# Kernel tuning notes

Hardware: AMD Instinct MI355X
Metric: run time of the kernel (lower is better)

The kernel has to match this reference:

```python
import jax, jax.numpy as jnp
from jax import lax
import numpy as np

ANCHOR_LENGTHS = (2.0, 4.0, 6.0, 9.0, 13.0, 18.0)  # A = 6


def make_anchors_1d(Lf, anchor_lengths):
    # anchors on the feature axis: [Lf*A, 2] (start, end)
    al = jnp.asarray(anchor_lengths, dtype=jnp.float32)          # [A]
    centers = jnp.arange(Lf, dtype=jnp.float32) + 0.5            # [Lf]
    start = centers[:, None] - 0.5 * al[None, :]                 # [Lf, A]
    end = centers[:, None] + 0.5 * al[None, :]                   # [Lf, A]
    return jnp.stack([start, end], axis=-1).reshape(Lf * al.shape[0], 2)


def setup_inputs() -> dict:
    key = jax.random.key(0)
    ks = jax.random.split(key, 4)
    B, C, Lf, A = 4, 512, 8192, len(ANCHOR_LENGTHS)
    feat = jax.random.normal(ks[0], (B, C, Lf), dtype=jnp.float32)
    conv_w = jax.random.normal(ks[1], (C, C, 3), dtype=jnp.float32) * 0.02   # OIW
    conv_b = jnp.zeros((C,), dtype=jnp.float32)
    obj_w = jax.random.normal(ks[2], (A, C, 1), dtype=jnp.float32) * 0.02
    obj_b = jnp.zeros((A,), dtype=jnp.float32)
    reg_w = jax.random.normal(ks[3], (A * 2, C, 1), dtype=jnp.float32) * 0.02
    reg_b = jnp.zeros((A * 2,), dtype=jnp.float32)
    return {"feat": feat, "conv_w": conv_w, "conv_b": conv_b,
            "obj_w": obj_w, "obj_b": obj_b, "reg_w": reg_w, "reg_b": reg_b}


def reference(feat, conv_w, conv_b, obj_w, obj_b, reg_w, reg_b):
    B, C, Lf = feat.shape
    A = obj_w.shape[0]
    # 3x1 conv, padding=1 -> SAME; layout N C W / O I W
    h = lax.conv_general_dilated(feat, conv_w, window_strides=(1,),
                                 padding="SAME",
                                 dimension_numbers=("NCH", "OIH", "NCH"))
    h = jax.nn.relu(h + conv_b[None, :, None])                   # [B, C, Lf]
    # 1x1 conv heads expressed as channel contractions
    obj = jnp.einsum("bcl,ac->bal", h, obj_w[:, :, 0]) + obj_b[None, :, None]   # [B, A, Lf]
    reg = jnp.einsum("bcl,ac->bal", h, reg_w[:, :, 0]) + reg_b[None, :, None]   # [B, 2A, Lf]
    obj = obj.transpose(0, 2, 1).reshape(B, Lf * A)                              # [B, N]
    reg = reg.transpose(0, 2, 1).reshape(B, Lf, A, 2).reshape(B, Lf * A, 2)      # [B, N, 2]
    anchors = make_anchors_1d(Lf, ANCHOR_LENGTHS)                                # [N, 2]
    return obj, reg, anchors
```

## Files before the change

### kernel.cpp

```cpp
#include <hip/hip_runtime.h>
#include <stdint.h>

typedef __attribute__((ext_vector_type(8))) short short8;
typedef __attribute__((ext_vector_type(4))) float f32x4;
typedef __attribute__((ext_vector_type(4))) float float4v;
typedef __attribute__((ext_vector_type(4))) unsigned short u16x4;
typedef __attribute__((ext_vector_type(8))) unsigned short u16x8;

#define AS1 __attribute__((address_space(1)))
#define AS3 __attribute__((address_space(3)))


__device__ __forceinline__ unsigned short f2bf(float f) {
    union { float f; unsigned int u; } v; v.f = f;
    unsigned int r = v.u + 0x7fffu + ((v.u >> 16) & 1u);
    return (unsigned short)(r >> 16);
}

__constant__ float c_AL[6] = {2.f, 4.f, 6.f, 9.f, 13.f, 18.f};

__global__ __launch_bounds__(256) void prep_transpose_kernel(
    const float* __restrict__ feat, const float* __restrict__ conv_w,
    const float* __restrict__ obj_w, const float* __restrict__ reg_w,
    unsigned short* __restrict__ wAf, unsigned short* __restrict__ hwp,
    unsigned short* __restrict__ featT, float* __restrict__ out) {
    __shared__ unsigned short tile[64][68];
    unsigned int bx = blockIdx.x;
    int tid = threadIdx.x;
    if (bx < 4096u) {
        int l0 = (bx & 127) * 64, c0 = ((bx >> 7) & 7) * 64, b = bx >> 10;
        const float* fb = feat + ((size_t)b * 512 + c0) * 8192 + l0;
        #pragma unroll
        for (int it = 0; it < 4; ++it) {
            int slot = it * 256 + tid;
            int c = slot >> 4, l4 = (slot & 15) << 2;
            float4v v = *(const float4v*)(fb + (size_t)c * 8192 + l4);
            u16x4 pk;
            pk.x = f2bf(v.x); pk.y = f2bf(v.y);
            pk.z = f2bf(v.z); pk.w = f2bf(v.w);
            *(u16x4*)(&tile[c][l4]) = pk;
        }
        __syncthreads();
        unsigned short* ftb = featT + ((size_t)b * 8208 + 1 + l0) * 512 + c0;
        #pragma unroll
        for (int it = 0; it < 2; ++it) {
            int slot = it * 256 + tid;
            int l = slot >> 3, c8 = (slot & 7) << 3;
            u16x8 pk;
            #pragma unroll
            for (int j = 0; j < 8; ++j) pk[j] = tile[c8 + j][l];
            *(u16x8*)(ftb + (size_t)l * 512 + c8) = pk;
        }
        return;
    }
    unsigned int idx = (bx - 4096u) * 256 + tid;
    if (idx < 786432u) {
        unsigned int chunkid = idx >> 9;
        unsigned int within = idx & 511u;
        unsigned int lane = within >> 3, j = within & 7u;
        unsigned int kc = chunkid & 15u;
        unsigned int ct = chunkid >> 4;
        unsigned int t = ct % 3u, cb = ct / 3u;
        unsigned int cout = cb * 16u + (lane & 15u);
        unsigned int cin = kc * 32u + (lane >> 4) * 8u + j;
        wAf[idx] = f2bf(conv_w[(cout * 512u + cin) * 3u + t]);
    } else if (idx < 802816u) {
        unsigned int i2 = idx - 786432u;
        unsigned int j = i2 >> 9, c = i2 & 511u;
        float v = 0.f;
        if (j < 6u) v = obj_w[j * 512u + c];
        else if (j < 18u) v = reg_w[(j - 6u) * 512u + c];
        hwp[i2] = f2bf(v);
    } else if (idx < 851968u) {
        unsigned int n = idx - 802816u;
        unsigned int l = n / 6u, a = n - l * 6u;
        float ctr = (float)l + 0.5f, half = 0.5f * c_AL[a];
        float* anchors = out + 589824;
        anchors[2 * n]     = ctr - half;
        anchors[2 * n + 1] = ctr + half;
    } else if (idx < 856064u) {
        unsigned int i4 = idx - 851968u;
        unsigned int b = i4 >> 10, rem = i4 & 1023u;
        unsigned int row = (rem >> 9) ? 8193u : 0u;
        unsigned int c = rem & 511u;
        featT[((size_t)b * 8208 + row) * 512 + c] = 0;
    }
}

__global__ __launch_bounds__(256, 4) void conv_gemm_kernel(
    const unsigned short* __restrict__ wAf,
    const unsigned short* __restrict__ featT,
    const float* __restrict__ conv_b,
    const unsigned short* __restrict__ hwp,
    float* __restrict__ part) {
    __shared__ unsigned short smem[17408];

    const int tid = threadIdx.x;
    const int wave = tid >> 6, lane = tid & 63;
    const int lq = lane >> 4, lr = lane & 15;
    const int l0 = blockIdx.x * 128;
    const int m0 = blockIdx.y * 128;
    const int b = blockIdx.z;
    const int wm = wave >> 1, wn = wave & 1;
    const unsigned short* ftb = featT + (size_t)b * 8208 * 512;

    f32x4 acc[4][4];
    #pragma unroll
    for (int i = 0; i < 4; ++i)
        #pragma unroll
        for (int j = 0; j < 4; ++j)
            acc[i][j] = (f32x4){0.f, 0.f, 0.f, 0.f};

    for (int kc = 0; kc < 16; ++kc) {
        __syncthreads();
        for (int ci = wave; ci < 33; ci += 4) {
            const unsigned short* g;
            if (ci < 24) {
                int t = ci >> 3, rb = ci & 7;
                g = wAf + ((size_t)(((m0 >> 4) + rb) * 3 + t) * 16 + kc) * 512 + lane * 8;
            } else {
                int lb = ci - 24;
                g = ftb + (size_t)(l0 + lb * 16 + lr) * 512 + kc * 32 + lq * 8;
            }
            __builtin_amdgcn_global_load_lds((const AS1 void*)g,
                                             (AS3 void*)(smem + ci * 512), 16, 0, 0);
        }
        __syncthreads();
        #pragma unroll
        for (int t = 0; t < 3; ++t) {
            short8 af[4], bf[4];
            #pragma unroll
            for (int fm = 0; fm < 4; ++fm)
                af[fm] = *(const short8*)(smem + ((t * 8 + wm * 4 + fm) << 9) + (lane << 3));
            #pragma unroll
            for (int fn = 0; fn < 4; ++fn) {
                int R = wn * 64 + fn * 16 + lr + t;
                bf[fn] = *(const short8*)(smem + ((24 + (R >> 4)) << 9) +
                                          ((((lq << 4) | (R & 15))) << 3));
            }
            #pragma unroll
            for (int fm = 0; fm < 4; ++fm)
                #pragma unroll
                for (int fn = 0; fn < 4; ++fn)
                    acc[fm][fn] = __builtin_amdgcn_mfma_f32_16x16x32_bf16(
                        af[fm], bf[fn], acc[fm][fn], 0, 0, 0);
        }
    }
    __syncthreads();
    #pragma unroll
    for (int fm = 0; fm < 4; ++fm) {
        int mb = wm * 64 + fm * 16 + lq * 4;
        float cb0 = conv_b[m0 + mb];
        float cb1 = conv_b[m0 + mb + 1];
        float cb2 = conv_b[m0 + mb + 2];
        float cb3 = conv_b[m0 + mb + 3];
        #pragma unroll
        for (int fn = 0; fn < 4; ++fn) {
            int n = wn * 64 + fn * 16 + lr;
            f32x4 v = acc[fm][fn];
            u16x4 pk;
            pk.x = f2bf(fmaxf(v.x + cb0, 0.f));
            pk.y = f2bf(fmaxf(v.y + cb1, 0.f));
            pk.z = f2bf(fmaxf(v.z + cb2, 0.f));
            pk.w = f2bf(fmaxf(v.w + cb3, 0.f));
            *(u16x4*)(smem + n * 136 + mb) = pk;
        }
    }
    __syncthreads();
    f32x4 hacc[2][2];
    #pragma unroll
    for (int i = 0; i < 2; ++i) {
        hacc[i][0] = (f32x4){0.f, 0.f, 0.f, 0.f};
        hacc[i][1] = (f32x4){0.f, 0.f, 0.f, 0.f};
    }
    const int lbase = wave * 32;
    for (int kk = 0; kk < 4; ++kk) {
        short8 ha[2], hb2[2];
        #pragma unroll
        for (int fm2 = 0; fm2 < 2; ++fm2)
            ha[fm2] = *(const short8*)(smem + (lbase + fm2 * 16 + lr) * 136 + kk * 32 + lq * 8);
        #pragma unroll
        for (int fn = 0; fn < 2; ++fn)
            hb2[fn] = *(const short8*)(hwp + (size_t)(fn * 16 + lr) * 512 + m0 + kk * 32 + lq * 8);
        #pragma unroll
        for (int fm2 = 0; fm2 < 2; ++fm2)
            #pragma unroll
            for (int fn = 0; fn < 2; ++fn)
                hacc[fm2][fn] = __builtin_amdgcn_mfma_f32_16x16x32_bf16(
                    ha[fm2], hb2[fn], hacc[fm2][fn], 0, 0, 0);
    }
    float* pb = part + ((size_t)(blockIdx.y * 4 + b) * 8192) * 18;
    #pragma unroll
    for (int fn = 0; fn < 2; ++fn) {
        int j = fn * 16 + lr;
        if (j >= 18) continue;
        #pragma unroll
        for (int fm2 = 0; fm2 < 2; ++fm2)
            #pragma unroll
            for (int r = 0; r < 4; ++r) {
                int l = l0 + lbase + fm2 * 16 + lq * 4 + r;
                pb[(size_t)l * 18 + j] = hacc[fm2][fn][r];
            }
    }
}

__global__ __launch_bounds__(256) void reduce_kernel(
    const float* __restrict__ part, const float* __restrict__ obj_b,
    const float* __restrict__ reg_b, float* __restrict__ out) {
    unsigned int idx = blockIdx.x * 256 + threadIdx.x;
    if (idx >= 589824u) return;
    unsigned int j = idx % 18u;
    unsigned int t = idx / 18u;
    unsigned int l = t & 8191u;
    unsigned int b = t >> 13;
    float s = 0.f;
    #pragma unroll
    for (int mb = 0; mb < 4; ++mb)
        s += part[((size_t)(mb * 4 + b) * 8192 + l) * 18 + j];
    if (j < 6u) {
        s += obj_b[j];
        out[(size_t)b * 49152 + l * 6 + j] = s;
    } else {
        s += reg_b[j - 6u];
        out[196608u + (size_t)b * 98304 + l * 12 + (j - 6u)] = s;
    }
}

extern "C" void kernel_launch(void* const* d_in, const int* in_sizes, int n_in,
                              void* d_out, int out_size, void* d_ws, size_t ws_size,
                              hipStream_t stream) {
    const float* feat   = (const float*)d_in[0];
    const float* conv_w = (const float*)d_in[1];
    const float* conv_b = (const float*)d_in[2];
    const float* obj_w  = (const float*)d_in[3];
    const float* obj_b  = (const float*)d_in[4];
    const float* reg_w  = (const float*)d_in[5];
    const float* reg_b  = (const float*)d_in[6];
    float* out = (float*)d_out;
    char* ws = (char*)d_ws;
    unsigned short* wAf   = (unsigned short*)(ws);
    unsigned short* hwp   = (unsigned short*)(ws + 1572864);
    unsigned short* featT = (unsigned short*)(ws + 1605632);
    float* part           = (float*)(ws + 35225600);

    prep_transpose_kernel<<<dim3(7440), dim3(256), 0, stream>>>(
        feat, conv_w, obj_w, reg_w, wAf, hwp, featT, out);
    conv_gemm_kernel<<<dim3(64, 4, 4), dim3(256), 0, stream>>>(wAf, featT, conv_b, hwp, part);
    reduce_kernel<<<dim3(2304), dim3(256), 0, stream>>>(part, obj_b, reg_b, out);
}
```

Before: 166.8 us.

## Fuse split-K reduction into GEMM via last-block atomic counter

Drops the separate reduce kernel. Each GEMM block now increments a per-(L-tile, batch) counter after writing its partial head outputs. The fourth block to arrive sums the four partials and writes obj/reg with bias. This removes one kernel launch and its extra pass over the partials, at the cost of a threadfence, an atomic per block and a serialized tail on the last-arriving block. Counters are zeroed in the prep kernel inside spare padding rows of the featT workspace.

```diff
diff --git a/kernel.cpp b/kernel.cpp
--- a/kernel.cpp
+++ b/kernel.cpp
@@ -23,7 +23,8 @@
     const float* __restrict__ feat, const float* __restrict__ conv_w,
     const float* __restrict__ obj_w, const float* __restrict__ reg_w,
     unsigned short* __restrict__ wAf, unsigned short* __restrict__ hwp,
-    unsigned short* __restrict__ featT, float* __restrict__ out) {
+    unsigned short* __restrict__ featT, unsigned int* __restrict__ cnt,
+    float* __restrict__ out) {
     __shared__ unsigned short tile[64][68];
     unsigned int bx = blockIdx.x;
     int tid = threadIdx.x;
@@ -84,6 +85,8 @@
         unsigned int row = (rem >> 9) ? 8193u : 0u;
         unsigned int c = rem & 511u;
         featT[((size_t)b * 8208 + row) * 512 + c] = 0;
+    } else if (idx < 856320u) {
+        cnt[idx - 856064u] = 0u;
     }
 }
 
@@ -92,7 +95,11 @@
     const unsigned short* __restrict__ featT,
     const float* __restrict__ conv_b,
     const unsigned short* __restrict__ hwp,
-    float* __restrict__ part) {
+    const float* __restrict__ obj_b,
+    const float* __restrict__ reg_b,
+    float* __restrict__ part,
+    unsigned int* __restrict__ cnt,
+    float* __restrict__ out) {
     __shared__ unsigned short smem[17408];
 
     const int tid = threadIdx.x;
@@ -202,27 +209,26 @@
                 pb[(size_t)l * 18 + j] = hacc[fm2][fn][r];
             }
     }
-}
-
-__global__ __launch_bounds__(256) void reduce_kernel(
-    const float* __restrict__ part, const float* __restrict__ obj_b,
-    const float* __restrict__ reg_b, float* __restrict__ out) {
-    unsigned int idx = blockIdx.x * 256 + threadIdx.x;
-    if (idx >= 589824u) return;
-    unsigned int j = idx % 18u;
-    unsigned int t = idx / 18u;
-    unsigned int l = t & 8191u;
-    unsigned int b = t >> 13;
-    float s = 0.f;
-    #pragma unroll
-    for (int mb = 0; mb < 4; ++mb)
-        s += part[((size_t)(mb * 4 + b) * 8192 + l) * 18 + j];
-    if (j < 6u) {
-        s += obj_b[j];
-        out[(size_t)b * 49152 + l * 6 + j] = s;
-    } else {
-        s += reg_b[j - 6u];
-        out[196608u + (size_t)b * 98304 + l * 12 + (j - 6u)] = s;
+    __threadfence();
+    __syncthreads();
+    volatile unsigned int* flag = (volatile unsigned int*)smem;
+    if (tid == 0)
+        *flag = atomicAdd(&cnt[blockIdx.x * 4 + b], 1u);
+    __syncthreads();
+    if (*flag == 3u) {
+        __threadfence();
+        float* outObj = out + (size_t)b * 49152;
+        float* outReg = out + 196608 + (size_t)b * 98304;
+        for (int i = tid; i < 2304; i += 256) {
+            int l = l0 + i / 18;
+            int j = i - (i / 18) * 18;
+            float s = 0.f;
+            #pragma unroll
+            for (int mb = 0; mb < 4; ++mb)
+                s += part[((size_t)(mb * 4 + b) * 8192 + l) * 18 + j];
+            if (j < 6) outObj[l * 6 + j] = s + obj_b[j];
+            else outReg[l * 12 + (j - 6)] = s + reg_b[j - 6];
+        }
     }
 }
 
@@ -242,9 +248,10 @@
     unsigned short* hwp   = (unsigned short*)(ws + 1572864);
     unsigned short* featT = (unsigned short*)(ws + 1605632);
     float* part           = (float*)(ws + 35225600);
-
-    prep_transpose_kernel<<<dim3(7440), dim3(256), 0, stream>>>(
-        feat, conv_w, obj_w, reg_w, wAf, hwp, featT, out);
-    conv_gemm_kernel<<<dim3(64, 4, 4), dim3(256), 0, stream>>>(wAf, featT, conv_b, hwp, part);
-    reduce_kernel<<<dim3(2304), dim3(256), 0, stream>>>(part, obj_b, reg_b, out);
-}
+    unsigned int* cnt = (unsigned int*)(featT + ((size_t)3 * 8208 + 8200) * 512);
+
+    prep_transpose_kernel<<<dim3(7441), dim3(256), 0, stream>>>(
+        feat, conv_w, obj_w, reg_w, wAf, hwp, featT, cnt, out);
+    conv_gemm_kernel<<<dim3(64, 4, 4), dim3(256), 0, stream>>>(
+        wAf, featT, conv_b, hwp, obj_b, reg_b, part, cnt, out);
+}
```

After: 329.2 us. 1.97x slower.
